# Optimization experiments

Measured on AMD Instinct MI355X. Metric: run time of the kernel, lower is better.

## Reference

```python
import jax, jax.numpy as jnp
import numpy as np

G = 16          # grid_size
U = 4           # num_controls
C = 4           # num_classes
B = 2048        # batch_size
HID = 64        # SegNet hidden channels (SegNet source unavailable; simple conv encoder assumed)
L = 1.0e6       # 'infinite' cost, matches C++ init g = 1e6
K = G * G       # value-iteration sweeps: upper bound on optimal path hop count
MOVES = [(-1, 0), (1, 0), (0, -1), (0, 1)]  # 4-connected controls


def conv2d(x, w, b):
    # x: (B,Cin,H,W), w: (Cout,Cin,3,3) SAME padding
    y = jax.lax.conv_general_dilated(x, w, (1, 1), 'SAME',
                                     dimension_numbers=('NCHW', 'OIHW', 'NCHW'))
    return y + b[None, :, None, None]


def neighbors(g):
    # g: (B,G,G) cost-to-go; returns (B,U,G,G) = g at x+move_u, L outside grid
    p = jnp.pad(g, ((0, 0), (1, 1), (1, 1)), constant_values=L)
    return jnp.stack([p[:, 1 + dr:1 + dr + G, 1 + dc:1 + dc + G] for dr, dc in MOVES], axis=1)


def shortest_path_Q(cost, loc, goal):
    # cost: (B,U,G,G) positive c(x,u); exact grid shortest-path via Bellman value iteration,
    # equivalent to the batched A* of the C++ extension.
    b_idx = jnp.arange(B)
    g0 = jnp.full((B, G, G), L, dtype=cost.dtype)
    g0 = g0.at[b_idx, goal[:, 0], goal[:, 1]].set(0.0)

    def step(g, _):
        g_new = jnp.minimum(g, jnp.min(cost + neighbors(g), axis=1))
        return g_new, None

    g, _ = jax.lax.scan(step, g0, None, length=K)
    Qmap = cost + neighbors(g)                       # (B,U,G,G): Q(x,u)
    # gather Q(start, u); loc in [1,G-1) so x+move stays on-grid
    return Qmap[b_idx[:, None], jnp.arange(U)[None, :], loc[:, 0:1], loc[:, 1:2]]


def setup_inputs() -> dict:
    key = jax.random.key(0)
    ks = jax.random.split(key, 6)
    grid_cnt = jax.random.uniform(ks[0], (B, C, G, G), dtype=jnp.float32) * 10.0
    loc = jax.random.randint(ks[1], (B, 2), 1, G - 1)
    goal = jax.random.randint(ks[2], (B, 2), 1, G - 1)
    theta = jnp.ones((C, G, G), dtype=jnp.float32)
    w1 = jax.random.normal(ks[3], (HID, C, 3, 3), dtype=jnp.float32) * 0.1
    b1 = jnp.zeros((HID,), dtype=jnp.float32)
    w2 = jax.random.normal(ks[4], (U, HID, 3, 3), dtype=jnp.float32) * 0.1
    b2 = jnp.zeros((U,), dtype=jnp.float32)
    return {"grid_cnt_batch": grid_cnt, "loc_batch": loc, "goal_batch": goal,
            "theta": theta, "w1": w1, "b1": b1, "w2": w2, "b2": b2}


def reference(grid_cnt_batch, loc_batch, goal_batch, theta, w1, b1, w2, b2):
    # map_encoder: per-pixel softmax over classes of grid_cnt * theta
    sem_prob = jax.nn.softmax(grid_cnt_batch * theta[None], axis=1)   # (B,C,G,G)
    # cost_encoder (SegNet stand-in): conv-relu-conv-softplus, strictly positive costs
    h = jax.nn.relu(conv2d(sem_prob, w1, b1))                          # (B,HID,G,G)
    cost = jax.nn.softplus(conv2d(h, w2, b2)) + 1e-6                   # (B,U,G,G)
    Q = shortest_path_Q(cost, loc_batch, goal_batch)                   # (B,U)
    logit = -Q
    return logit, jax.nn.softmax(logit, axis=1)
```

## Files before the change

### kernel.cpp

```cpp
#include <hip/hip_runtime.h>
#include <math.h>

#define GSZ   16
#define NPIX  256
#define LBIG  1.0e6f
#define PW    18
#define PP18  324
#define HBS   (PP18 * 16)

typedef __fp16 f16x8 __attribute__((ext_vector_type(8)));
typedef __fp16 h2v   __attribute__((ext_vector_type(2)));
typedef float  f32x4 __attribute__((ext_vector_type(4)));
union UH2 { unsigned u; h2v h; };
union F8U { f16x8 h; uint4 u; unsigned w[4]; };
union UF  { unsigned u; float f; };

__device__ __forceinline__ unsigned pk2(float a, float b) {
    UH2 u; u.h = __builtin_amdgcn_cvt_pkrtz(a, b);
    return u.u;
}
__device__ __forceinline__ unsigned pk2relu(float a, float b) {
    UH2 u; u.h = __builtin_amdgcn_cvt_pkrtz(a, b);
    h2v z = { (__fp16)0.0f, (__fp16)0.0f };
    u.h = __builtin_elementwise_max(u.h, z);
    return u.u;
}
__device__ __forceinline__ float dpp_up1(float x) {
    UF s; s.f = x; UF r;
    r.u = (unsigned)__builtin_amdgcn_update_dpp(0, (int)s.u, 0x111, 0xF, 0xF, true);
    return r.f;
}
__device__ __forceinline__ float dpp_dn1(float x) {
    UF s; s.f = x; UF r;
    r.u = (unsigned)__builtin_amdgcn_update_dpp(0, (int)s.u, 0x101, 0xF, 0xF, true);
    return r.f;
}

__global__ void pack_weights(const float* __restrict__ w1,
                             const float* __restrict__ w2,
                             __fp16* __restrict__ pw) {
    int i = blockIdx.x * 256 + threadIdx.x;
    if (i < 4096) {
        int j = i & 7, lane = (i >> 3) & 63, t = i >> 9;
        int ks = t >> 2, nt = t & 3;
        int oc = nt * 16 + (lane & 15);
        int k  = ks * 32 + ((lane >> 4) & 3) * 8 + j;
        int tap = k >> 2, cls = k & 3;
        pw[i] = (tap < 9) ? (__fp16)w1[oc * 36 + cls * 9 + tap] : (__fp16)0.0f;
    } else if (i < 4096 + 9216) {
        int m = i - 4096;
        int j = m & 7, lane = (m >> 3) & 63, t = m >> 9;
        int ks = t & 1, tap = t >> 1;
        int u  = lane & 15;
        int oc = ks * 32 + ((lane >> 4) & 3) * 8 + j;
        pw[i] = (u < 4) ? (__fp16)w2[u * 576 + oc * 9 + tap] : (__fp16)0.0f;
    }
}

__device__ __forceinline__ int ring_idx(int t) {
    return (t < 18) ? t
         : (t < 36) ? (306 + (t - 18))
         : (t < 52) ? ((t - 35) * PW)
                    : ((t - 51) * PW + 17);
}

__global__ __launch_bounds__(256, 2) void semirl_kernel(
    const float*  __restrict__ grid_cnt,
    const int*    __restrict__ loc,
    const int*    __restrict__ goal,
    const float*  __restrict__ theta,
    const float*  __restrict__ b1,
    const float*  __restrict__ b2,
    const __fp16* __restrict__ pw,
    float*        __restrict__ out,
    int B)
{
    const int b0   = blockIdx.x * 4;
    const int tid  = threadIdx.x;
    const int lane = tid & 63;
    const int wv   = tid >> 6;
    const int g    = (lane >> 4) & 3;
    const int ln   = lane & 15;

    __shared__ uint2 s_sem[PP18];
    __shared__ uint4 s_h4[8 * PP18];
    __shared__ uint2 s_costh[4][NPIX];
    char*  s_hb   = (char*)s_h4;
    float* s_gout = (float*)s_h4;

    F8U w1f[2][4];
    {
        const uint4* p1 = (const uint4*)pw;
        #pragma unroll
        for (int ks = 0; ks < 2; ++ks)
            #pragma unroll
            for (int nt = 0; nt < 4; ++nt)
                w1f[ks][nt].u = p1[(ks * 4 + nt) * 64 + lane];
    }
    F8U w2f[9][2];
    {
        const uint4* p2 = (const uint4*)(pw + 4096);
        #pragma unroll
        for (int tp = 0; tp < 9; ++tp)
            #pragma unroll
            for (int ks = 0; ks < 2; ++ks)
                w2f[tp][ks].u = p2[(tp * 2 + ks) * 64 + lane];
    }
    float4 bias1v[4];
    #pragma unroll
    for (int nt = 0; nt < 4; ++nt)
        bias1v[nt] = *(const float4*)&b1[nt * 16 + g * 4];
    const float4 b2v = *(const float4*)b2;

    const int eidx = b0 + wv;
    const int grr = goal[2 * eidx], gcc = goal[2 * eidx + 1];
    const int lr  = loc[2 * eidx],  lc  = loc[2 * eidx + 1];

    float th[4], gi[4][4];
    #pragma unroll
    for (int c = 0; c < 4; ++c) th[c] = theta[c * NPIX + tid];
    #pragma unroll
    for (int e = 0; e < 4; ++e)
        #pragma unroll
        for (int c = 0; c < 4; ++c)
            gi[e][c] = grid_cnt[(size_t)(b0 + e) * (4 * NPIX) + c * NPIX + tid];

    if (tid < 68) s_sem[ring_idx(tid)] = make_uint2(0u, 0u);
    for (int i2 = tid; i2 < 544; i2 += 256) {
        int qq = ring_idx(i2 >> 3);
        s_h4[(i2 & 7) * PP18 + qq] = make_uint4(0u, 0u, 0u, 0u);
    }
    const int pr = tid >> 4, pc = tid & 15;
    {
        float x0 = gi[0][0] * th[0], x1 = gi[0][1] * th[1];
        float x2 = gi[0][2] * th[2], x3 = gi[0][3] * th[3];
        float m  = fmaxf(fmaxf(x0, x1), fmaxf(x2, x3));
        float e0 = __expf(x0 - m), e1 = __expf(x1 - m);
        float e2 = __expf(x2 - m), e3 = __expf(x3 - m);
        float inv = 1.0f / (e0 + e1 + e2 + e3);
        s_sem[(pr + 1) * PW + (pc + 1)] =
            make_uint2(pk2(e0 * inv, e1 * inv), pk2(e2 * inv, e3 * inv));
    }
    __syncthreads();

    const int off0 = (g == 0) ? (-PW - 1) : (g == 1) ? (-PW + 1) : (g == 2) ? 0 : (PW - 1);
    const int off1 = (g == 0) ? (-PW)     : (g == 1) ? (-1)      : (g == 2) ? 1 : PW;
    const int OFF[9] = { -PW - 1, -PW, -PW + 1, -1, 0, 1, PW - 1, PW, PW + 1 };

    #pragma unroll
    for (int e = 0; e < 4; ++e) {
        #pragma unroll
        for (int i = 0; i < 4; ++i) {
            const int mt = wv * 4 + i;
            const int pp = (mt + 1) * PW + (ln + 1);
            const uint2 A0 = s_sem[pp + off0];
            const uint2 A1 = s_sem[pp + off1];
            const uint2 A2 = s_sem[pp + (PW + 1)];
            F8U a0, a1;
            a0.w[0] = A0.x; a0.w[1] = A0.y; a0.w[2] = A1.x; a0.w[3] = A1.y;
            a1.w[0] = A2.x; a1.w[1] = A2.y; a1.w[2] = 0u;  a1.w[3] = 0u;
            char* wbase = s_hb + (g >> 1) * HBS + pp * 16 + (g & 1) * 8;
            #pragma unroll
            for (int nt = 0; nt < 4; ++nt) {
                f32x4 acc = { bias1v[nt].x, bias1v[nt].y, bias1v[nt].z, bias1v[nt].w };
                acc = __builtin_amdgcn_mfma_f32_16x16x32_f16(w1f[0][nt].h, a0.h, acc, 0, 0, 0);
                acc = __builtin_amdgcn_mfma_f32_16x16x32_f16(w1f[1][nt].h, a1.h, acc, 0, 0, 0);
                uint2 hv;
                hv.x = pk2relu(acc[0], acc[1]);
                hv.y = pk2relu(acc[2], acc[3]);
                *(uint2*)(wbase + nt * (2 * HBS)) = hv;
            }
        }
        __syncthreads();

        #pragma unroll
        for (int i = 0; i < 4; ++i) {
            const int mt = wv * 4 + i;
            const int pp = (mt + 1) * PW + (ln + 1);
            const char* hb0 = s_hb + g * HBS + pp * 16;
            const char* hb1 = hb0 + 4 * HBS;
            f32x4 cacc0, cacc1;
            cacc0[0] = (g == 0) ? b2v.x : 0.0f;
            cacc0[1] = (g == 0) ? b2v.y : 0.0f;
            cacc0[2] = (g == 0) ? b2v.z : 0.0f;
            cacc0[3] = (g == 0) ? b2v.w : 0.0f;
            cacc1[0] = 0.0f; cacc1[1] = 0.0f; cacc1[2] = 0.0f; cacc1[3] = 0.0f;
            #pragma unroll
            for (int tp = 0; tp < 9; ++tp) {
                F8U af0, af1;
                af0.u = *(const uint4*)(hb0 + OFF[tp] * 16);
                af1.u = *(const uint4*)(hb1 + OFF[tp] * 16);
                cacc0 = __builtin_amdgcn_mfma_f32_16x16x32_f16(w2f[tp][0].h, af0.h, cacc0, 0, 0, 0);
                cacc1 = __builtin_amdgcn_mfma_f32_16x16x32_f16(w2f[tp][1].h, af1.h, cacc1, 0, 0, 0);
            }
            if (g == 0) {
                float x0 = cacc0[0] + cacc1[0];
                float x1 = cacc0[1] + cacc1[1];
                float x2 = cacc0[2] + cacc1[2];
                float x3 = cacc0[3] + cacc1[3];
                float c0s = fmaxf(x0, 0.0f) + __logf(1.0f + __expf(-fabsf(x0))) + 1e-6f;
                float c1s = fmaxf(x1, 0.0f) + __logf(1.0f + __expf(-fabsf(x1))) + 1e-6f;
                float c2s = fmaxf(x2, 0.0f) + __logf(1.0f + __expf(-fabsf(x2))) + 1e-6f;
                float c3s = fmaxf(x3, 0.0f) + __logf(1.0f + __expf(-fabsf(x3))) + 1e-6f;
                s_costh[e][mt * 16 + ln] = make_uint2(pk2(c0s, c1s), pk2(c2s, c3s));
            }
        }
        if (e < 3) {
            float x0 = gi[e+1][0] * th[0], x1 = gi[e+1][1] * th[1];
            float x2 = gi[e+1][2] * th[2], x3 = gi[e+1][3] * th[3];
            float m  = fmaxf(fmaxf(x0, x1), fmaxf(x2, x3));
            float e0 = __expf(x0 - m), e1 = __expf(x1 - m);
            float e2 = __expf(x2 - m), e3 = __expf(x3 - m);
            float inv = 1.0f / (e0 + e1 + e2 + e3);
            s_sem[(pr + 1) * PW + (pc + 1)] =
                make_uint2(pk2(e0 * inv, e1 * inv), pk2(e2 * inv, e3 * inv));
        }
        __syncthreads();
    }

    {
        const int cv  = ln;
        const int rgv = g;
        const int r0  = rgv * 4;

        float cs[4][4];
        #pragma unroll
        for (int i = 0; i < 4; ++i) {
            const uint2 cw = s_costh[wv][(r0 + i) * GSZ + cv];
            UH2 a, bq; a.u = cw.x; bq.u = cw.y;
            cs[i][0] = (float)a.h[0];  cs[i][1] = (float)a.h[1];
            cs[i][2] = (float)bq.h[0]; cs[i][3] = (float)bq.h[1];
        }
        if (cv == 0)  { cs[0][2] = LBIG; cs[1][2] = LBIG; cs[2][2] = LBIG; cs[3][2] = LBIG; }
        if (cv == 15) { cs[0][3] = LBIG; cs[1][3] = LBIG; cs[2][3] = LBIG; cs[3][3] = LBIG; }
        if (rgv == 0) cs[0][0] = LBIG;
        if (rgv == 3) cs[3][1] = LBIG;

        float gg[4];
        #pragma unroll
        for (int i = 0; i < 4; ++i)
            gg[i] = (cv == gcc && (r0 + i) == grr) ? 0.0f : LBIG;

        for (int k = 0; k < 128; ++k) {
            const float gu = __shfl_up(gg[3], 16);
            const float gd = __shfl_down(gg[0], 16);
            bool ch = false;
            #pragma unroll
            for (int s = 0; s < 2; ++s) {
                float lf[4], rt[4];
                #pragma unroll
                for (int i = 0; i < 4; ++i) { lf[i] = dpp_up1(gg[i]); rt[i] = dpp_dn1(gg[i]); }
                const float up[4] = { gu, gg[0], gg[1], gg[2] };
                const float dn[4] = { gg[1], gg[2], gg[3], gd };
                #pragma unroll
                for (int i = 0; i < 4; ++i) {
                    float s0 = cs[i][0] + up[i];
                    float s1 = cs[i][1] + dn[i];
                    float s2 = cs[i][2] + lf[i];
                    float s3 = cs[i][3] + rt[i];
                    float q  = fminf(fminf(fminf(s0, s1), s2), fminf(s3, gg[i]));
                    ch = ch || (q < gg[i]);
                    gg[i] = q;
                }
            }
            if (__ballot(ch) == 0ULL) break;
        }

        #pragma unroll
        for (int i = 0; i < 4; ++i)
            s_gout[wv * NPIX + (r0 + i) * GSZ + cv] = gg[i];
    }

    if (lane == 0) {
        const int lp = lr * GSZ + lc;
        const uint2 cw = s_costh[wv][lp];
        UH2 a, bq; a.u = cw.x; bq.u = cw.y;
        float Q0 = (float)a.h[0]  + s_gout[wv * NPIX + lp - GSZ];
        float Q1 = (float)a.h[1]  + s_gout[wv * NPIX + lp + GSZ];
        float Q2 = (float)bq.h[0] + s_gout[wv * NPIX + lp - 1];
        float Q3 = (float)bq.h[1] + s_gout[wv * NPIX + lp + 1];
        float l0 = -Q0, l1 = -Q1, l2 = -Q2, l3 = -Q3;
        float m  = fmaxf(fmaxf(l0, l1), fmaxf(l2, l3));
        float e0 = __expf(l0 - m), e1 = __expf(l1 - m);
        float e2 = __expf(l2 - m), e3 = __expf(l3 - m);
        float inv = 1.0f / (e0 + e1 + e2 + e3);
        float* lo = out + (size_t)eidx * 4;
        float* po = out + (size_t)B * 4 + (size_t)eidx * 4;
        lo[0] = l0; lo[1] = l1; lo[2] = l2; lo[3] = l3;
        po[0] = e0 * inv; po[1] = e1 * inv; po[2] = e2 * inv; po[3] = e3 * inv;
    }
}

extern "C" void kernel_launch(void* const* d_in, const int* in_sizes, int n_in,
                              void* d_out, int out_size, void* d_ws, size_t ws_size,
                              hipStream_t stream) {
    const float* grid_cnt = (const float*)d_in[0];
    const int*   loc      = (const int*)  d_in[1];
    const int*   goal     = (const int*)  d_in[2];
    const float* theta    = (const float*)d_in[3];
    const float* w1       = (const float*)d_in[4];
    const float* b1       = (const float*)d_in[5];
    const float* w2       = (const float*)d_in[6];
    const float* b2       = (const float*)d_in[7];
    float*       outp     = (float*)d_out;
    __fp16*      pw       = (__fp16*)d_ws;
    const int B = in_sizes[1] / 2;

    hipLaunchKernelGGL(pack_weights, dim3(52), dim3(256), 0, stream, w1, w2, pw);
    hipLaunchKernelGGL(semirl_kernel, dim3(B / 4), dim3(256), 0, stream,
                       grid_cnt, loc, goal, theta, b1, b2, pw, outp, B);
}
```

Baseline: 31.89 us.

## Give each wave a private hidden-feature tile with halo rows to drop block barriers

Each wave now computes conv1 for its own 4 output rows plus one halo row above and below, into a wave-private LDS buffer. Conv2 can then read that buffer without the two block-wide barriers per batch element. Softmax for all four batch elements is computed up front into separate semantic buffers, and the per-element loop is no longer unrolled. In exchange, conv1 MFMA work grows by about 1.5x through the redundant halo rows, and LDS use rises to roughly 74KB per block, which could affect occupancy.

```diff
diff --git a/kernel.cpp b/kernel.cpp
--- a/kernel.cpp
+++ b/kernel.cpp
@@ -6,7 +6,10 @@
 #define LBIG  1.0e6f
 #define PW    18
 #define PP18  324
-#define HBS   (PP18 * 16)
+#define SROW  6
+#define SPP   (SROW * 18)
+#define HBW   (SPP * 16)
+#define HWV   (8 * HBW)
 
 typedef __fp16 f16x8 __attribute__((ext_vector_type(8)));
 typedef __fp16 h2v   __attribute__((ext_vector_type(2)));
@@ -82,11 +85,12 @@
     const int g    = (lane >> 4) & 3;
     const int ln   = lane & 15;
 
-    __shared__ uint2 s_sem[PP18];
-    __shared__ uint4 s_h4[8 * PP18];
+    __shared__ uint2 s_semAll[4 * PP18];
+    __shared__ uint4 s_hw[4 * 8 * SPP];
     __shared__ uint2 s_costh[4][NPIX];
-    char*  s_hb   = (char*)s_h4;
-    float* s_gout = (float*)s_h4;
+    char* s_hb = (char*)s_hw;
+    char* hpriv = s_hb + wv * HWV;
+    float* s_gout_w = (float*)hpriv;
 
     F8U w1f[2][4];
     {
@@ -125,20 +129,25 @@
         for (int c = 0; c < 4; ++c)
             gi[e][c] = grid_cnt[(size_t)(b0 + e) * (4 * NPIX) + c * NPIX + tid];
 
-    if (tid < 68) s_sem[ring_idx(tid)] = make_uint2(0u, 0u);
-    for (int i2 = tid; i2 < 544; i2 += 256) {
-        int qq = ring_idx(i2 >> 3);
-        s_h4[(i2 & 7) * PP18 + qq] = make_uint4(0u, 0u, 0u, 0u);
+    {
+        uint4* hz = (uint4*)hpriv;
+        const uint4 z4 = make_uint4(0u, 0u, 0u, 0u);
+        for (int j = lane; j < 8 * SPP; j += 64) hz[j] = z4;
+    }
+    for (int j = tid; j < 4 * 68; j += 256) {
+        int e = j / 68, t = j % 68;
+        s_semAll[e * PP18 + ring_idx(t)] = make_uint2(0u, 0u);
     }
     const int pr = tid >> 4, pc = tid & 15;
-    {
-        float x0 = gi[0][0] * th[0], x1 = gi[0][1] * th[1];
-        float x2 = gi[0][2] * th[2], x3 = gi[0][3] * th[3];
+    #pragma unroll
+    for (int e = 0; e < 4; ++e) {
+        float x0 = gi[e][0] * th[0], x1 = gi[e][1] * th[1];
+        float x2 = gi[e][2] * th[2], x3 = gi[e][3] * th[3];
         float m  = fmaxf(fmaxf(x0, x1), fmaxf(x2, x3));
         float e0 = __expf(x0 - m), e1 = __expf(x1 - m);
         float e2 = __expf(x2 - m), e3 = __expf(x3 - m);
         float inv = 1.0f / (e0 + e1 + e2 + e3);
-        s_sem[(pr + 1) * PW + (pc + 1)] =
+        s_semAll[e * PP18 + (pr + 1) * PW + (pc + 1)] =
             make_uint2(pk2(e0 * inv, e1 * inv), pk2(e2 * inv, e3 * inv));
     }
     __syncthreads();
@@ -147,19 +156,21 @@
     const int off1 = (g == 0) ? (-PW)     : (g == 1) ? (-1)      : (g == 2) ? 1 : PW;
     const int OFF[9] = { -PW - 1, -PW, -PW + 1, -1, 0, 1, PW - 1, PW, PW + 1 };
 
-    #pragma unroll
+    #pragma unroll 1
     for (int e = 0; e < 4; ++e) {
-        #pragma unroll
-        for (int i = 0; i < 4; ++i) {
-            const int mt = wv * 4 + i;
-            const int pp = (mt + 1) * PW + (ln + 1);
-            const uint2 A0 = s_sem[pp + off0];
-            const uint2 A1 = s_sem[pp + off1];
-            const uint2 A2 = s_sem[pp + (PW + 1)];
+        const uint2* semE = s_semAll + e * PP18;
+        #pragma unroll
+        for (int rr = 0; rr < SROW; ++rr) {
+            const int r = wv * 4 - 1 + rr;
+            if ((unsigned)r > 15u) continue;
+            const int spp = (r + 1) * PW + (ln + 1);
+            const uint2 A0 = semE[spp + off0];
+            const uint2 A1 = semE[spp + off1];
+            const uint2 A2 = semE[spp + (PW + 1)];
             F8U a0, a1;
             a0.w[0] = A0.x; a0.w[1] = A0.y; a0.w[2] = A1.x; a0.w[3] = A1.y;
             a1.w[0] = A2.x; a1.w[1] = A2.y; a1.w[2] = 0u;  a1.w[3] = 0u;
-            char* wbase = s_hb + (g >> 1) * HBS + pp * 16 + (g & 1) * 8;
+            char* wbase = hpriv + (g >> 1) * HBW + (rr * 18 + ln + 1) * 16 + (g & 1) * 8;
             #pragma unroll
             for (int nt = 0; nt < 4; ++nt) {
                 f32x4 acc = { bias1v[nt].x, bias1v[nt].y, bias1v[nt].z, bias1v[nt].w };
@@ -168,17 +179,15 @@
                 uint2 hv;
                 hv.x = pk2relu(acc[0], acc[1]);
                 hv.y = pk2relu(acc[2], acc[3]);
-                *(uint2*)(wbase + nt * (2 * HBS)) = hv;
+                *(uint2*)(wbase + nt * (2 * HBW)) = hv;
             }
         }
-        __syncthreads();
-
         #pragma unroll
         for (int i = 0; i < 4; ++i) {
-            const int mt = wv * 4 + i;
-            const int pp = (mt + 1) * PW + (ln + 1);
-            const char* hb0 = s_hb + g * HBS + pp * 16;
-            const char* hb1 = hb0 + 4 * HBS;
+            const int mt  = wv * 4 + i;
+            const int lpp = (i + 1) * 18 + (ln + 1);
+            const char* hb0 = hpriv + g * HBW + lpp * 16;
+            const char* hb1 = hb0 + 4 * HBW;
             f32x4 cacc0, cacc1;
             cacc0[0] = (g == 0) ? b2v.x : 0.0f;
             cacc0[1] = (g == 0) ? b2v.y : 0.0f;
@@ -205,18 +214,8 @@
                 s_costh[e][mt * 16 + ln] = make_uint2(pk2(c0s, c1s), pk2(c2s, c3s));
             }
         }
-        if (e < 3) {
-            float x0 = gi[e+1][0] * th[0], x1 = gi[e+1][1] * th[1];
-            float x2 = gi[e+1][2] * th[2], x3 = gi[e+1][3] * th[3];
-            float m  = fmaxf(fmaxf(x0, x1), fmaxf(x2, x3));
-            float e0 = __expf(x0 - m), e1 = __expf(x1 - m);
-            float e2 = __expf(x2 - m), e3 = __expf(x3 - m);
-            float inv = 1.0f / (e0 + e1 + e2 + e3);
-            s_sem[(pr + 1) * PW + (pc + 1)] =
-                make_uint2(pk2(e0 * inv, e1 * inv), pk2(e2 * inv, e3 * inv));
-        }
-        __syncthreads();
-    }
+    }
+    __syncthreads();
 
     {
         const int cv  = ln;
@@ -268,17 +267,17 @@
 
         #pragma unroll
         for (int i = 0; i < 4; ++i)
-            s_gout[wv * NPIX + (r0 + i) * GSZ + cv] = gg[i];
+            s_gout_w[(r0 + i) * GSZ + cv] = gg[i];
     }
 
     if (lane == 0) {
         const int lp = lr * GSZ + lc;
         const uint2 cw = s_costh[wv][lp];
         UH2 a, bq; a.u = cw.x; bq.u = cw.y;
-        float Q0 = (float)a.h[0]  + s_gout[wv * NPIX + lp - GSZ];
-        float Q1 = (float)a.h[1]  + s_gout[wv * NPIX + lp + GSZ];
-        float Q2 = (float)bq.h[0] + s_gout[wv * NPIX + lp - 1];
-        float Q3 = (float)bq.h[1] + s_gout[wv * NPIX + lp + 1];
+        float Q0 = (float)a.h[0]  + s_gout_w[lp - GSZ];
+        float Q1 = (float)a.h[1]  + s_gout_w[lp + GSZ];
+        float Q2 = (float)bq.h[0] + s_gout_w[lp - 1];
+        float Q3 = (float)bq.h[1] + s_gout_w[lp + 1];
         float l0 = -Q0, l1 = -Q1, l2 = -Q2, l3 = -Q3;
         float m  = fmaxf(fmaxf(l0, l1), fmaxf(l2, l3));
         float e0 = __expf(l0 - m), e1 = __expf(l1 - m);
```

New measurement: 32.78 us. 1.03x slower.

## Replace Jacobi Bellman sweeps with directional prefix-scan relaxations

Applied to the files above, without the earlier changes.

Replaces the local 4-neighbor Bellman relaxation with directional sweeps (down, up, right, left). Each sweep is computed as a min-plus prefix scan along rows and columns, using in-register chains, cross-lane shuffles and DPP row shifts. Information can then propagate across the whole grid per round, cutting the number of rounds needed to converge. The trade-off is more instructions per round and longer dependency chains in the scans, and edge handling now depends on lane-index masks instead of LBIG-patched costs.

```diff
diff --git a/kernel.cpp b/kernel.cpp
--- a/kernel.cpp
+++ b/kernel.cpp
@@ -25,14 +25,10 @@
     u.h = __builtin_elementwise_max(u.h, z);
     return u.u;
 }
-__device__ __forceinline__ float dpp_up1(float x) {
+template<int CTRL>
+__device__ __forceinline__ float dppf(float x) {
     UF s; s.f = x; UF r;
-    r.u = (unsigned)__builtin_amdgcn_update_dpp(0, (int)s.u, 0x111, 0xF, 0xF, true);
-    return r.f;
-}
-__device__ __forceinline__ float dpp_dn1(float x) {
-    UF s; s.f = x; UF r;
-    r.u = (unsigned)__builtin_amdgcn_update_dpp(0, (int)s.u, 0x101, 0xF, 0xF, true);
+    r.u = (unsigned)__builtin_amdgcn_update_dpp(0, (int)s.u, CTRL, 0xF, 0xF, true);
     return r.f;
 }
 
@@ -231,38 +227,87 @@
             cs[i][0] = (float)a.h[0];  cs[i][1] = (float)a.h[1];
             cs[i][2] = (float)bq.h[0]; cs[i][3] = (float)bq.h[1];
         }
-        if (cv == 0)  { cs[0][2] = LBIG; cs[1][2] = LBIG; cs[2][2] = LBIG; cs[3][2] = LBIG; }
-        if (cv == 15) { cs[0][3] = LBIG; cs[1][3] = LBIG; cs[2][3] = LBIG; cs[3][3] = LBIG; }
-        if (rgv == 0) cs[0][0] = LBIG;
-        if (rgv == 3) cs[3][1] = LBIG;
 
         float gg[4];
         #pragma unroll
         for (int i = 0; i < 4; ++i)
             gg[i] = (cv == gcc && (r0 + i) == grr) ? 0.0f : LBIG;
 
-        for (int k = 0; k < 128; ++k) {
-            const float gu = __shfl_up(gg[3], 16);
-            const float gd = __shfl_down(gg[0], 16);
-            bool ch = false;
-            #pragma unroll
-            for (int s = 0; s < 2; ++s) {
-                float lf[4], rt[4];
+        for (int round = 0; round < 64; ++round) {
+            const float o0 = gg[0], o1 = gg[1], o2 = gg[2], o3 = gg[3];
+
+            {
+                float p0 = gg[0];                              float s0 = cs[0][0];
+                float p1 = fminf(gg[1], cs[1][0] + p0);        float s1 = cs[1][0] + s0;
+                float p2 = fminf(gg[2], cs[2][0] + p1);        float s2 = cs[2][0] + s1;
+                float p3 = fminf(gg[3], cs[3][0] + p2);        float s3 = cs[3][0] + s2;
+                const float P = __shfl_up(p3, 16);
+                const float S = __shfl_up(s3, 16);
+                float T = LBIG;
                 #pragma unroll
-                for (int i = 0; i < 4; ++i) { lf[i] = dpp_up1(gg[i]); rt[i] = dpp_dn1(gg[i]); }
-                const float up[4] = { gu, gg[0], gg[1], gg[2] };
-                const float dn[4] = { gg[1], gg[2], gg[3], gd };
+                for (int it = 0; it < 3; ++it) {
+                    float Tup = __shfl_up(T, 16);
+                    T = (rgv == 0) ? LBIG : fminf(P, Tup + S);
+                }
+                gg[0] = fminf(p0, T + s0);
+                gg[1] = fminf(p1, T + s1);
+                gg[2] = fminf(p2, T + s2);
+                gg[3] = fminf(p3, T + s3);
+            }
+            {
+                float p3 = gg[3];                              float s3 = cs[3][1];
+                float p2 = fminf(gg[2], cs[2][1] + p3);        float s2 = cs[2][1] + s3;
+                float p1 = fminf(gg[1], cs[1][1] + p2);        float s1 = cs[1][1] + s2;
+                float p0 = fminf(gg[0], cs[0][1] + p1);        float s0 = cs[0][1] + s1;
+                const float P = __shfl_down(p0, 16);
+                const float S = __shfl_down(s0, 16);
+                float T = LBIG;
                 #pragma unroll
-                for (int i = 0; i < 4; ++i) {
-                    float s0 = cs[i][0] + up[i];
-                    float s1 = cs[i][1] + dn[i];
-                    float s2 = cs[i][2] + lf[i];
-                    float s3 = cs[i][3] + rt[i];
-                    float q  = fminf(fminf(fminf(s0, s1), s2), fminf(s3, gg[i]));
-                    ch = ch || (q < gg[i]);
-                    gg[i] = q;
+                for (int it = 0; it < 3; ++it) {
+                    float Tdn = __shfl_down(T, 16);
+                    T = (rgv == 3) ? LBIG : fminf(P, Tdn + S);
                 }
-            }
+                gg[3] = fminf(p3, T + s3);
+                gg[2] = fminf(p2, T + s2);
+                gg[1] = fminf(p1, T + s1);
+                gg[0] = fminf(p0, T + s0);
+            }
+            #pragma unroll
+            for (int i = 0; i < 4; ++i) {
+                float v = gg[i], w = cs[i][2];
+                { float sv = dppf<0x111>(v), sw = dppf<0x111>(w);
+                  sv = (cv >= 1) ? sv : LBIG; sw = (cv >= 1) ? sw : 0.0f;
+                  float nv = fminf(v, sv + w); w = sw + w; v = nv; }
+                { float sv = dppf<0x112>(v), sw = dppf<0x112>(w);
+                  sv = (cv >= 2) ? sv : LBIG; sw = (cv >= 2) ? sw : 0.0f;
+                  float nv = fminf(v, sv + w); w = sw + w; v = nv; }
+                { float sv = dppf<0x114>(v), sw = dppf<0x114>(w);
+                  sv = (cv >= 4) ? sv : LBIG; sw = (cv >= 4) ? sw : 0.0f;
+                  float nv = fminf(v, sv + w); w = sw + w; v = nv; }
+                { float sv = dppf<0x118>(v);
+                  sv = (cv >= 8) ? sv : LBIG;
+                  v = fminf(v, sv + w); }
+                gg[i] = v;
+            }
+            #pragma unroll
+            for (int i = 0; i < 4; ++i) {
+                float v = gg[i], w = cs[i][3];
+                { float sv = dppf<0x101>(v), sw = dppf<0x101>(w);
+                  sv = (cv <= 14) ? sv : LBIG; sw = (cv <= 14) ? sw : 0.0f;
+                  float nv = fminf(v, sv + w); w = sw + w; v = nv; }
+                { float sv = dppf<0x102>(v), sw = dppf<0x102>(w);
+                  sv = (cv <= 13) ? sv : LBIG; sw = (cv <= 13) ? sw : 0.0f;
+                  float nv = fminf(v, sv + w); w = sw + w; v = nv; }
+                { float sv = dppf<0x104>(v), sw = dppf<0x104>(w);
+                  sv = (cv <= 11) ? sv : LBIG; sw = (cv <= 11) ? sw : 0.0f;
+                  float nv = fminf(v, sv + w); w = sw + w; v = nv; }
+                { float sv = dppf<0x108>(v);
+                  sv = (cv <= 7) ? sv : LBIG;
+                  v = fminf(v, sv + w); }
+                gg[i] = v;
+            }
+
+            const bool ch = (gg[0] < o0) || (gg[1] < o1) || (gg[2] < o2) || (gg[3] < o3);
             if (__ballot(ch) == 0ULL) break;
         }
 
```

Result: slower. 36.84 us (+15.5%).
